# Optimization experiments

Hardware: AMD Instinct MI355X
Metric: run time of the kernel (lower is better)

The kernel has to match this reference:

```python
import jax, jax.numpy as jnp
import numpy as np

DIM = 512
HEADS = 8
DIM_HEAD = 64
DIM_INNER = HEADS * DIM_HEAD  # 512
SCALE = DIM_HEAD ** -0.5


def setup_inputs() -> dict:
    key = jax.random.key(0)
    k1, k2, k3 = jax.random.split(key, 3)
    x = jax.random.normal(k1, (8, 2048, DIM), dtype=jnp.float32)
    # Linear weights (no bias). Stored as [in, out] for x @ W.
    w_qkv = jax.random.normal(k2, (DIM, 3 * DIM_INNER), dtype=jnp.float32) * (DIM ** -0.5)
    w_out = jax.random.normal(k3, (DIM_INNER, DIM), dtype=jnp.float32) * (DIM_INNER ** -0.5)
    return {"x": x, "w_qkv": w_qkv, "w_out": w_out}


def reference(x, w_qkv, w_out):
    b, n, _ = x.shape
    qkv = x @ w_qkv  # [b, n, 3*h*d]
    qkv = qkv.reshape(b, n, 3, HEADS, DIM_HEAD)
    qkv = jnp.transpose(qkv, (2, 0, 3, 1, 4))  # [3, b, h, n, d]
    q, k, v = qkv[0], qkv[1], qkv[2]
    q = q * SCALE
    sim = jnp.einsum('bhid,bhjd->bhij', q, k)
    attn = jax.nn.softmax(sim, axis=-1)
    out = jnp.einsum('bhij,bhjd->bhid', attn, v)  # [b, h, n, d]
    out = jnp.transpose(out, (0, 2, 1, 3)).reshape(b, n, DIM_INNER)
    return out @ w_out
```

## Files before the change

kernel.cpp:

```cpp
#include <hip/hip_runtime.h>
#include <hip/hip_bf16.h>
#include <stdint.h>


#define NB 8
#define SEQ 2048
#define DIMM 512
#define HEADS 8
#define DHEAD 64
#define MTOT (NB * SEQ)

typedef __attribute__((ext_vector_type(8))) short bf16x8;
typedef __attribute__((ext_vector_type(4))) float f32x4;
typedef __attribute__((ext_vector_type(16))) float f32x16;
typedef __attribute__((ext_vector_type(4))) uint u32x4;

__device__ __forceinline__ ushort f2b(float f) {
  union { float f; uint32_t u; } c; c.f = f;
  return (ushort)((c.u + 0x7FFFu + ((c.u >> 16) & 1u)) >> 16);
}

__device__ __forceinline__ uint cvtpk(float lo, float hi) {
  uint r;
  asm("v_cvt_pk_bf16_f32 %0, %1, %2" : "=v"(r) : "v"(lo), "v"(hi));
  return r;
}
__device__ __forceinline__ void plswap(uint& a, uint& b) {
  asm("v_permlane32_swap_b32 %0, %1" : "+v"(a), "+v"(b));
}
__device__ __forceinline__ bf16x8 mk8(uint a, uint b, uint c, uint d) {
  u32x4 t = {a, b, c, d};
  return __builtin_bit_cast(bf16x8, t);
}

__global__ void cvt_bf16(const float* __restrict__ src, ushort* __restrict__ dst, int n8) {
  int i = blockIdx.x * blockDim.x + threadIdx.x;
  if (i >= n8) return;
  const float4* s = (const float4*)src;
  float4 a = s[2 * i], b = s[2 * i + 1];
  ushort o[8] = {f2b(a.x), f2b(a.y), f2b(a.z), f2b(a.w),
                 f2b(b.x), f2b(b.y), f2b(b.z), f2b(b.w)};
  *(uint4*)(dst + 8 * i) = *(const uint4*)o;
}

__global__ void cvt_transpose(const float* __restrict__ src, ushort* __restrict__ dst,
                              int R, int C) {
  __shared__ ushort tile[64][72];
  int nbc = C >> 6;
  int bc = blockIdx.x % nbc, br = blockIdx.x / nbc;
  int c0 = bc * 64, r0 = br * 64;
  #pragma unroll
  for (int p = 0; p < 16; ++p) {
    int e = p * 256 + threadIdx.x;
    int r = e >> 6, c = e & 63;
    tile[r][c] = f2b(src[(size_t)(r0 + r) * C + c0 + c]);
  }
  __syncthreads();
  #pragma unroll
  for (int p = 0; p < 16; ++p) {
    int e = p * 256 + threadIdx.x;
    int ct = e >> 6, rt = e & 63;
    dst[(size_t)(c0 + ct) * R + r0 + rt] = tile[rt][ct];
  }
}

__global__ __launch_bounds__(256) void gemm_qkv(
    const ushort* __restrict__ A, const ushort* __restrict__ Bt,
    ushort* __restrict__ qo, ushort* __restrict__ ko, ushort* __restrict__ vto) {
  __shared__ ushort As[128][72];
  __shared__ ushort Bs[128][72];
  const int tid = threadIdx.x;
  const int bn = blockIdx.x % 12, bm = blockIdx.x / 12;
  const int wid = tid >> 6, lane = tid & 63;
  const int wm = (wid >> 1) * 64, wn = (wid & 1) * 64;
  const int lr = lane & 15, lk = (lane >> 4) * 8;

  f32x4 acc[4][4] = {};
  const ushort* Ab = A + (size_t)(bm * 128) * DIMM;
  const ushort* Bb = Bt + (size_t)(bn * 128) * DIMM;

  for (int kt = 0; kt < DIMM; kt += 64) {
    __syncthreads();
    #pragma unroll
    for (int p = 0; p < 4; ++p) {
      int e = p * 256 + tid;
      int r = e >> 3, c8 = (e & 7) << 3;
      *(uint4*)&As[r][c8] = *(const uint4*)(Ab + (size_t)r * DIMM + kt + c8);
      *(uint4*)&Bs[r][c8] = *(const uint4*)(Bb + (size_t)r * DIMM + kt + c8);
    }
    __syncthreads();
    #pragma unroll
    for (int kk = 0; kk < 64; kk += 32) {
      bf16x8 af[4], bfr[4];
      #pragma unroll
      for (int i = 0; i < 4; ++i) af[i] = *(const bf16x8*)&As[wm + i * 16 + lr][kk + lk];
      #pragma unroll
      for (int j = 0; j < 4; ++j) bfr[j] = *(const bf16x8*)&Bs[wn + j * 16 + lr][kk + lk];
      #pragma unroll
      for (int i = 0; i < 4; ++i)
        #pragma unroll
        for (int j = 0; j < 4; ++j)
          acc[i][j] = __builtin_amdgcn_mfma_f32_16x16x32_bf16(af[i], bfr[j], acc[i][j], 0, 0, 0);
    }
  }

  const int rb = bm * 128 + wm + ((lane >> 4) << 2);
  const int cb = bn * 128 + wn + lr;
  const float QSCALE = 0.125f * 1.44269504f;
  #pragma unroll
  for (int i = 0; i < 4; ++i) {
    #pragma unroll
    for (int j = 0; j < 4; ++j) {
      int col = cb + j * 16;
      int t = col >> 9, h = (col >> 6) & 7, d = col & 63;
      f32x4 v = acc[i][j];
      #pragma unroll
      for (int e = 0; e < 4; ++e) {
        int row = rb + i * 16 + e;
        int b = row >> 11, n = row & 2047;
        float val = v[e];
        if (t == 0) {
          qo[(((size_t)b * HEADS + h) * SEQ + n) * DHEAD + d] = f2b(val * QSCALE);
        } else if (t == 1) {
          ko[(((size_t)b * HEADS + h) * SEQ + n) * DHEAD + d] = f2b(val);
        } else {
          vto[(((size_t)b * HEADS + h) * DHEAD + d) * SEQ + n] = f2b(val);
        }
      }
    }
  }
}

__global__ __launch_bounds__(256) void gemm_out(
    const ushort* __restrict__ A, const ushort* __restrict__ Bt, float* __restrict__ out) {
  __shared__ ushort As[128][72];
  __shared__ ushort Bs[128][72];
  const int tid = threadIdx.x;
  const int bn = blockIdx.x % 4, bm = blockIdx.x / 4;
  const int wid = tid >> 6, lane = tid & 63;
  const int wm = (wid >> 1) * 64, wn = (wid & 1) * 64;
  const int lr = lane & 15, lk = (lane >> 4) * 8;

  f32x4 acc[4][4] = {};
  const ushort* Ab = A + (size_t)(bm * 128) * DIMM;
  const ushort* Bb = Bt + (size_t)(bn * 128) * DIMM;

  for (int kt = 0; kt < DIMM; kt += 64) {
    __syncthreads();
    #pragma unroll
    for (int p = 0; p < 4; ++p) {
      int e = p * 256 + tid;
      int r = e >> 3, c8 = (e & 7) << 3;
      *(uint4*)&As[r][c8] = *(const uint4*)(Ab + (size_t)r * DIMM + kt + c8);
      *(uint4*)&Bs[r][c8] = *(const uint4*)(Bb + (size_t)r * DIMM + kt + c8);
    }
    __syncthreads();
    #pragma unroll
    for (int kk = 0; kk < 64; kk += 32) {
      bf16x8 af[4], bfr[4];
      #pragma unroll
      for (int i = 0; i < 4; ++i) af[i] = *(const bf16x8*)&As[wm + i * 16 + lr][kk + lk];
      #pragma unroll
      for (int j = 0; j < 4; ++j) bfr[j] = *(const bf16x8*)&Bs[wn + j * 16 + lr][kk + lk];
      #pragma unroll
      for (int i = 0; i < 4; ++i)
        #pragma unroll
        for (int j = 0; j < 4; ++j)
          acc[i][j] = __builtin_amdgcn_mfma_f32_16x16x32_bf16(af[i], bfr[j], acc[i][j], 0, 0, 0);
    }
  }

  const int rb = bm * 128 + wm + ((lane >> 4) << 2);
  const int cb = bn * 128 + wn + lr;
  #pragma unroll
  for (int i = 0; i < 4; ++i)
    #pragma unroll
    for (int j = 0; j < 4; ++j) {
      f32x4 v = acc[i][j];
      #pragma unroll
      for (int e = 0; e < 4; ++e)
        out[(size_t)(rb + i * 16 + e) * DIMM + cb + j * 16] = v[e];
    }
}

__global__ __launch_bounds__(256) void attn(
    const ushort* __restrict__ q, const ushort* __restrict__ k,
    const ushort* __restrict__ vt, ushort* __restrict__ ao) {
  __shared__ ushort Ks[64 * 64];
  __shared__ ushort Vs[64 * 64];

  const int tid = threadIdx.x;
  const int wid = tid >> 6, l = tid & 63;
  const int l31 = l & 31, hi = l >> 5;
  const int bh = blockIdx.x >> 4, qb = blockIdx.x & 15;
  const ushort* kb = k + (size_t)bh * SEQ * DHEAD;
  const ushort* vb = vt + (size_t)bh * DHEAD * SEQ;
  const int nq = qb * 128 + wid * 32 + l31;

  bf16x8 qf[4];
  const ushort* qrow = q + (size_t)bh * SEQ * DHEAD + (size_t)nq * DHEAD;
  #pragma unroll
  for (int ks = 0; ks < 4; ++ks)
    qf[ks] = *(const bf16x8*)(qrow + ks * 16 + hi * 8);

  f32x16 accO0 = {}, accO1 = {};
  float mrun = -1e30f, lrun = 0.f;

  const int sr = tid >> 3, sc = tid & 7;
  const int swz = (sc ^ (sr & 7)) << 3;
  uint4 k0 = *(const uint4*)(kb + (size_t)sr * DHEAD + sc * 8);
  uint4 k1 = *(const uint4*)(kb + (size_t)(sr + 32) * DHEAD + sc * 8);
  uint4 v0 = *(const uint4*)(vb + (size_t)sr * SEQ + sc * 8);
  uint4 v1 = *(const uint4*)(vb + (size_t)(sr + 32) * SEQ + sc * 8);

  const int fsx = (l31 & 7);

  for (int t = 0; t < SEQ / 64; ++t) {
    __syncthreads();
    *(uint4*)&Ks[sr * 64 + swz] = k0;
    *(uint4*)&Ks[(sr + 32) * 64 + swz] = k1;
    *(uint4*)&Vs[sr * 64 + swz] = v0;
    *(uint4*)&Vs[(sr + 32) * 64 + swz] = v1;
    __syncthreads();

    if (t + 1 < SEQ / 64) {
      int nt = (t + 1) * 64;
      k0 = *(const uint4*)(kb + (size_t)(nt + sr) * DHEAD + sc * 8);
      k1 = *(const uint4*)(kb + (size_t)(nt + sr + 32) * DHEAD + sc * 8);
      v0 = *(const uint4*)(vb + (size_t)sr * SEQ + nt + sc * 8);
      v1 = *(const uint4*)(vb + (size_t)(sr + 32) * SEQ + nt + sc * 8);
    }

    f32x16 s0 = {}, s1 = {};
    #pragma unroll
    for (int ks = 0; ks < 4; ++ks) {
      int g = (ks << 1) | hi;
      int so = (g ^ fsx) << 3;
      bf16x8 kf0 = *(const bf16x8*)&Ks[l31 * 64 + so];
      bf16x8 kf1 = *(const bf16x8*)&Ks[(32 + l31) * 64 + so];
      s0 = __builtin_amdgcn_mfma_f32_32x32x16_bf16(kf0, qf[ks], s0, 0, 0, 0);
      s1 = __builtin_amdgcn_mfma_f32_32x32x16_bf16(kf1, qf[ks], s1, 0, 0, 0);
    }

    float mx = s0[0];
    #pragma unroll
    for (int i = 1; i < 16; ++i) mx = fmaxf(mx, s0[i]);
    #pragma unroll
    for (int i = 0; i < 16; ++i) mx = fmaxf(mx, s1[i]);
    mx = fmaxf(mx, __shfl_xor(mx, 32));

    if (__any(mx - mrun > 8.0f)) {
      float mnew = fmaxf(mrun, mx);
      float alpha = __builtin_amdgcn_exp2f(mrun - mnew);
      mrun = mnew;
      lrun *= alpha;
      #pragma unroll
      for (int i = 0; i < 16; ++i) { accO0[i] *= alpha; accO1[i] *= alpha; }
    }

    float rs = 0.f;
    #pragma unroll
    for (int i = 0; i < 16; ++i) {
      s0[i] = __builtin_amdgcn_exp2f(s0[i] - mrun); rs += s0[i];
      s1[i] = __builtin_amdgcn_exp2f(s1[i] - mrun); rs += s1[i];
    }
    rs += __shfl_xor(rs, 32);
    lrun += rs;

    bf16x8 pf0, pf1, pf2, pf3;
    {
      uint a0 = cvtpk(s0[0], s0[1]),  a1 = cvtpk(s0[2], s0[3]);
      uint b0 = cvtpk(s0[4], s0[5]),  b1 = cvtpk(s0[6], s0[7]);
      plswap(a0, b0); plswap(a1, b1);
      pf0 = mk8(a0, a1, b0, b1);
      a0 = cvtpk(s0[8], s0[9]);   a1 = cvtpk(s0[10], s0[11]);
      b0 = cvtpk(s0[12], s0[13]); b1 = cvtpk(s0[14], s0[15]);
      plswap(a0, b0); plswap(a1, b1);
      pf1 = mk8(a0, a1, b0, b1);
      a0 = cvtpk(s1[0], s1[1]);   a1 = cvtpk(s1[2], s1[3]);
      b0 = cvtpk(s1[4], s1[5]);   b1 = cvtpk(s1[6], s1[7]);
      plswap(a0, b0); plswap(a1, b1);
      pf2 = mk8(a0, a1, b0, b1);
      a0 = cvtpk(s1[8], s1[9]);   a1 = cvtpk(s1[10], s1[11]);
      b0 = cvtpk(s1[12], s1[13]); b1 = cvtpk(s1[14], s1[15]);
      plswap(a0, b0); plswap(a1, b1);
      pf3 = mk8(a0, a1, b0, b1);
    }

    #pragma unroll
    for (int kk = 0; kk < 4; ++kk) {
      int g = (kk << 1) | hi;
      int so = (g ^ fsx) << 3;
      bf16x8 vf0 = *(const bf16x8*)&Vs[l31 * 64 + so];
      bf16x8 vf1 = *(const bf16x8*)&Vs[(32 + l31) * 64 + so];
      bf16x8 pk = (kk == 0) ? pf0 : (kk == 1) ? pf1 : (kk == 2) ? pf2 : pf3;
      accO0 = __builtin_amdgcn_mfma_f32_32x32x16_bf16(vf0, pk, accO0, 0, 0, 0);
      accO1 = __builtin_amdgcn_mfma_f32_32x32x16_bf16(vf1, pk, accO1, 0, 0, 0);
    }
  }

  const int b = bh >> 3, h = bh & 7;
  const float rl = 1.0f / lrun;
  ushort* aop = ao + ((size_t)b * SEQ + nq) * DIMM + h * DHEAD;
  #pragma unroll
  for (int gq = 0; gq < 4; ++gq) {
    {
      int d0 = 8 * gq + 4 * hi;
      uint u0 = (uint)f2b(accO0[4 * gq + 0] * rl) | ((uint)f2b(accO0[4 * gq + 1] * rl) << 16);
      uint u1 = (uint)f2b(accO0[4 * gq + 2] * rl) | ((uint)f2b(accO0[4 * gq + 3] * rl) << 16);
      *(uint2*)(aop + d0) = make_uint2(u0, u1);
    }
    {
      int d0 = 32 + 8 * gq + 4 * hi;
      uint u0 = (uint)f2b(accO1[4 * gq + 0] * rl) | ((uint)f2b(accO1[4 * gq + 1] * rl) << 16);
      uint u1 = (uint)f2b(accO1[4 * gq + 2] * rl) | ((uint)f2b(accO1[4 * gq + 3] * rl) << 16);
      *(uint2*)(aop + d0) = make_uint2(u0, u1);
    }
  }
}

extern "C" void kernel_launch(void* const* d_in, const int* in_sizes, int n_in,
                              void* d_out, int out_size, void* d_ws, size_t ws_size,
                              hipStream_t stream) {
  const float* x = (const float*)d_in[0];
  const float* wqkv = (const float*)d_in[1];
  const float* wout = (const float*)d_in[2];
  float* out = (float*)d_out;

  char* ws = (char*)d_ws;
  const size_t SZ = (size_t)MTOT * DIMM * 2;
  ushort* xb    = (ushort*)(ws);
  ushort* qw    = (ushort*)(ws + SZ);
  ushort* kw    = (ushort*)(ws + 2 * SZ);
  ushort* vtw   = (ushort*)(ws + 3 * SZ);
  ushort* aow   = (ushort*)(ws + 4 * SZ);
  ushort* wqkvT = (ushort*)(ws + 5 * SZ);
  ushort* woutT = (ushort*)(ws + 5 * SZ + (size_t)1536 * 512 * 2);

  hipLaunchKernelGGL(cvt_bf16, dim3(4096), dim3(256), 0, stream, x, xb, MTOT * DIMM / 8);
  hipLaunchKernelGGL(cvt_transpose, dim3(192), dim3(256), 0, stream, wqkv, wqkvT, 512, 1536);
  hipLaunchKernelGGL(cvt_transpose, dim3(64), dim3(256), 0, stream, wout, woutT, 512, 512);
  hipLaunchKernelGGL(gemm_qkv, dim3(128 * 12), dim3(256), 0, stream, xb, wqkvT, qw, kw, vtw);
  hipLaunchKernelGGL(attn, dim3(64 * 16), dim3(256), 0, stream, qw, kw, vtw, aow);
  hipLaunchKernelGGL(gemm_out, dim3(128 * 4), dim3(256), 0, stream, aow, woutT, out);
}
```

Baseline: 201.1 us.

## Double-buffer K/V tiles in LDS with one barrier per iteration

Moves the attention kernel from a single K/V LDS buffer with two barriers per tile to ping-pong buffers. The next tile's LDS store happens after the QK^T MFMAs, and global prefetch now runs two tiles ahead, so the loop needs only one __syncthreads. It also turns the row max and row sum into tree reductions to shorten dependency chains, and raises wave priority with s_setprio around the MFMA blocks. LDS use doubles to 32KB per block, which could lower occupancy, and the extra in-flight registers add pressure.

```diff
diff --git a/kernel.cpp b/kernel.cpp
--- a/kernel.cpp
+++ b/kernel.cpp
@@ -186,8 +186,8 @@
 __global__ __launch_bounds__(256) void attn(
     const ushort* __restrict__ q, const ushort* __restrict__ k,
     const ushort* __restrict__ vt, ushort* __restrict__ ao) {
-  __shared__ ushort Ks[64 * 64];
-  __shared__ ushort Vs[64 * 64];
+  __shared__ ushort Ks0[64 * 64], Vs0[64 * 64];
+  __shared__ ushort Ks1[64 * 64], Vs1[64 * 64];
 
   const int tid = threadIdx.x;
   const int wid = tid >> 6, l = tid & 63;
@@ -208,46 +208,60 @@
 
   const int sr = tid >> 3, sc = tid & 7;
   const int swz = (sc ^ (sr & 7)) << 3;
+
   uint4 k0 = *(const uint4*)(kb + (size_t)sr * DHEAD + sc * 8);
   uint4 k1 = *(const uint4*)(kb + (size_t)(sr + 32) * DHEAD + sc * 8);
   uint4 v0 = *(const uint4*)(vb + (size_t)sr * SEQ + sc * 8);
   uint4 v1 = *(const uint4*)(vb + (size_t)(sr + 32) * SEQ + sc * 8);
-
-  const int fsx = (l31 & 7);
-
-  for (int t = 0; t < SEQ / 64; ++t) {
-    __syncthreads();
-    *(uint4*)&Ks[sr * 64 + swz] = k0;
-    *(uint4*)&Ks[(sr + 32) * 64 + swz] = k1;
-    *(uint4*)&Vs[sr * 64 + swz] = v0;
-    *(uint4*)&Vs[(sr + 32) * 64 + swz] = v1;
-    __syncthreads();
-
-    if (t + 1 < SEQ / 64) {
-      int nt = (t + 1) * 64;
+  *(uint4*)&Ks0[sr * 64 + swz] = k0;  *(uint4*)&Ks0[(sr + 32) * 64 + swz] = k1;
+  *(uint4*)&Vs0[sr * 64 + swz] = v0;  *(uint4*)&Vs0[(sr + 32) * 64 + swz] = v1;
+  k0 = *(const uint4*)(kb + (size_t)(64 + sr) * DHEAD + sc * 8);
+  k1 = *(const uint4*)(kb + (size_t)(64 + sr + 32) * DHEAD + sc * 8);
+  v0 = *(const uint4*)(vb + (size_t)sr * SEQ + 64 + sc * 8);
+  v1 = *(const uint4*)(vb + (size_t)(sr + 32) * SEQ + 64 + sc * 8);
+
+  const ushort* cK = Ks0; const ushort* cV = Vs0;
+  ushort* nK = Ks1;       ushort* nV = Vs1;
+
+  const int fx = l31 & 7;
+
+  for (int t = 0; t < 32; ++t) {
+    __syncthreads();
+
+    f32x16 s0 = {}, s1 = {};
+    __builtin_amdgcn_s_setprio(1);
+    #pragma unroll
+    for (int ks = 0; ks < 4; ++ks) {
+      const int so = ((2 * ks + hi) ^ fx) << 3;
+      bf16x8 kf0 = *(const bf16x8*)(cK + l31 * 64 + so);
+      bf16x8 kf1 = *(const bf16x8*)(cK + (32 + l31) * 64 + so);
+      s0 = __builtin_amdgcn_mfma_f32_32x32x16_bf16(kf0, qf[ks], s0, 0, 0, 0);
+      s1 = __builtin_amdgcn_mfma_f32_32x32x16_bf16(kf1, qf[ks], s1, 0, 0, 0);
+    }
+    __builtin_amdgcn_s_setprio(0);
+
+    if (t < 31) {
+      *(uint4*)(nK + sr * 64 + swz) = k0;
+      *(uint4*)(nK + (sr + 32) * 64 + swz) = k1;
+      *(uint4*)(nV + sr * 64 + swz) = v0;
+      *(uint4*)(nV + (sr + 32) * 64 + swz) = v1;
+    }
+    if (t < 30) {
+      int nt = (t + 2) * 64;
       k0 = *(const uint4*)(kb + (size_t)(nt + sr) * DHEAD + sc * 8);
       k1 = *(const uint4*)(kb + (size_t)(nt + sr + 32) * DHEAD + sc * 8);
       v0 = *(const uint4*)(vb + (size_t)sr * SEQ + nt + sc * 8);
       v1 = *(const uint4*)(vb + (size_t)(sr + 32) * SEQ + nt + sc * 8);
     }
 
-    f32x16 s0 = {}, s1 = {};
-    #pragma unroll
-    for (int ks = 0; ks < 4; ++ks) {
-      int g = (ks << 1) | hi;
-      int so = (g ^ fsx) << 3;
-      bf16x8 kf0 = *(const bf16x8*)&Ks[l31 * 64 + so];
-      bf16x8 kf1 = *(const bf16x8*)&Ks[(32 + l31) * 64 + so];
-      s0 = __builtin_amdgcn_mfma_f32_32x32x16_bf16(kf0, qf[ks], s0, 0, 0, 0);
-      s1 = __builtin_amdgcn_mfma_f32_32x32x16_bf16(kf1, qf[ks], s1, 0, 0, 0);
-    }
-
-    float mx = s0[0];
-    #pragma unroll
-    for (int i = 1; i < 16; ++i) mx = fmaxf(mx, s0[i]);
-    #pragma unroll
-    for (int i = 0; i < 16; ++i) mx = fmaxf(mx, s1[i]);
-    mx = fmaxf(mx, __shfl_xor(mx, 32));
+    float red[16];
+    #pragma unroll
+    for (int i = 0; i < 16; ++i) red[i] = fmaxf(s0[i], s1[i]);
+    #pragma unroll
+    for (int st = 8; st > 0; st >>= 1)
+      #pragma unroll
+      for (int i = 0; i < st; ++i) red[i] = fmaxf(red[i], red[i + st]);
+    float mx = fmaxf(red[0], __shfl_xor(red[0], 32));
 
     if (__any(mx - mrun > 8.0f)) {
       float mnew = fmaxf(mrun, mx);
@@ -258,45 +272,52 @@
       for (int i = 0; i < 16; ++i) { accO0[i] *= alpha; accO1[i] *= alpha; }
     }
 
-    float rs = 0.f;
     #pragma unroll
     for (int i = 0; i < 16; ++i) {
-      s0[i] = __builtin_amdgcn_exp2f(s0[i] - mrun); rs += s0[i];
-      s1[i] = __builtin_amdgcn_exp2f(s1[i] - mrun); rs += s1[i];
-    }
-    rs += __shfl_xor(rs, 32);
-    lrun += rs;
-
-    bf16x8 pf0, pf1, pf2, pf3;
+      s0[i] = __builtin_amdgcn_exp2f(s0[i] - mrun);
+      s1[i] = __builtin_amdgcn_exp2f(s1[i] - mrun);
+    }
+    #pragma unroll
+    for (int i = 0; i < 16; ++i) red[i] = s0[i] + s1[i];
+    #pragma unroll
+    for (int st = 8; st > 0; st >>= 1)
+      #pragma unroll
+      for (int i = 0; i < st; ++i) red[i] += red[i + st];
+    lrun += red[0] + __shfl_xor(red[0], 32);
+
+    bf16x8 pf[4];
     {
       uint a0 = cvtpk(s0[0], s0[1]),  a1 = cvtpk(s0[2], s0[3]);
       uint b0 = cvtpk(s0[4], s0[5]),  b1 = cvtpk(s0[6], s0[7]);
       plswap(a0, b0); plswap(a1, b1);
-      pf0 = mk8(a0, a1, b0, b1);
+      pf[0] = mk8(a0, a1, b0, b1);
       a0 = cvtpk(s0[8], s0[9]);   a1 = cvtpk(s0[10], s0[11]);
       b0 = cvtpk(s0[12], s0[13]); b1 = cvtpk(s0[14], s0[15]);
       plswap(a0, b0); plswap(a1, b1);
-      pf1 = mk8(a0, a1, b0, b1);
+      pf[1] = mk8(a0, a1, b0, b1);
       a0 = cvtpk(s1[0], s1[1]);   a1 = cvtpk(s1[2], s1[3]);
       b0 = cvtpk(s1[4], s1[5]);   b1 = cvtpk(s1[6], s1[7]);
       plswap(a0, b0); plswap(a1, b1);
-      pf2 = mk8(a0, a1, b0, b1);
+      pf[2] = mk8(a0, a1, b0, b1);
       a0 = cvtpk(s1[8], s1[9]);   a1 = cvtpk(s1[10], s1[11]);
       b0 = cvtpk(s1[12], s1[13]); b1 = cvtpk(s1[14], s1[15]);
       plswap(a0, b0); plswap(a1, b1);
-      pf3 = mk8(a0, a1, b0, b1);
-    }
-
+      pf[3] = mk8(a0, a1, b0, b1);
+    }
+
+    __builtin_amdgcn_s_setprio(1);
     #pragma unroll
     for (int kk = 0; kk < 4; ++kk) {
-      int g = (kk << 1) | hi;
-      int so = (g ^ fsx) << 3;
-      bf16x8 vf0 = *(const bf16x8*)&Vs[l31 * 64 + so];
-      bf16x8 vf1 = *(const bf16x8*)&Vs[(32 + l31) * 64 + so];
-      bf16x8 pk = (kk == 0) ? pf0 : (kk == 1) ? pf1 : (kk == 2) ? pf2 : pf3;
-      accO0 = __builtin_amdgcn_mfma_f32_32x32x16_bf16(vf0, pk, accO0, 0, 0, 0);
-      accO1 = __builtin_amdgcn_mfma_f32_32x32x16_bf16(vf1, pk, accO1, 0, 0, 0);
-    }
+      const int so = ((2 * kk + hi) ^ fx) << 3;
+      bf16x8 vf0 = *(const bf16x8*)(cV + l31 * 64 + so);
+      bf16x8 vf1 = *(const bf16x8*)(cV + (32 + l31) * 64 + so);
+      accO0 = __builtin_amdgcn_mfma_f32_32x32x16_bf16(vf0, pf[kk], accO0, 0, 0, 0);
+      accO1 = __builtin_amdgcn_mfma_f32_32x32x16_bf16(vf1, pf[kk], accO1, 0, 0, 0);
+    }
+    __builtin_amdgcn_s_setprio(0);
+
+    const ushort* tK = cK; cK = nK; nK = (ushort*)tK;
+    const ushort* tV = cV; cV = nV; nV = (ushort*)tV;
   }
 
   const int b = bh >> 3, h = bh & 7;
```

New measurement: 212.2 us. +5.5%, slower.
